# Kernel optimization log

Measured on AMD Instinct MI355X. Metric: run time of the kernel, lower is better.

The kernel has to match this reference:

```python
import jax, jax.numpy as jnp
import numpy as np

ALPHA = 0.2  # LeakyReLU negative slope
NEG_BIG = jnp.float32(-9e15)


def _leaky_relu(x):
    return jnp.where(x > 0, x, ALPHA * x)


def gat_layer(h, adj, w, a):
    """One GATLayer with concat=True (ELU output), dropout=0 (eval mode).
    h: [N, F_in], adj: [N, N] int, w: [F_in, F_out], a: [2*F_out, 1].
    """
    Wh = h @ w                         # [N, F_out]
    f_out = w.shape[1]
    Wh1 = Wh @ a[:f_out]               # [N, 1]
    Wh2 = Wh @ a[f_out:]               # [N, 1]
    e = _leaky_relu(Wh1 + Wh2.T)       # [N, N] dense additive scores
    att = jnp.where(adj > 0, e, NEG_BIG)
    att = jax.nn.softmax(att, axis=1)  # row softmax
    return jax.nn.elu(att @ Wh)        # [N, F_out]


def setup_inputs() -> dict:
    N, F_IN, H, NHEADS = 4096, 128, 64, 4
    key = jax.random.key(0)
    ks = jax.random.split(key, 9)
    s = jnp.float32(0.1)  # keep logits in a sane range
    x = jax.random.normal(ks[0], (N, F_IN), jnp.float32)
    adj = jax.random.randint(ks[1], (N, N), 0, 2, jnp.int32)
    return {
        "x": x,
        "adj": adj,
        "w_heads": jax.random.normal(ks[2], (NHEADS, F_IN, H), jnp.float32) * s,
        "a_heads": jax.random.normal(ks[3], (NHEADS, 2 * H, 1), jnp.float32) * s,
        "w_out": jax.random.normal(ks[4], (NHEADS * H, H), jnp.float32) * s,
        "a_out": jax.random.normal(ks[5], (2 * H, 1), jnp.float32) * s,
        "lin_w": jax.random.normal(ks[6], (H, F_IN), jnp.float32) * s,
        "lin_b": jnp.zeros((H,), jnp.float32),
        "outlin_w": jax.random.normal(ks[7], (H, H), jnp.float32) * s,
        "outlin_b": jnp.zeros((H,), jnp.float32),
    }


def reference(x, adj, w_heads, a_heads, w_out, a_out, lin_w, lin_b, outlin_w, outlin_b):
    N = x.shape[0]
    x_residual = x @ lin_w.T + lin_b                      # nn.Linear(input, hidden)
    # multi-head GAT layers, concatenated along features
    heads = jax.vmap(gat_layer, in_axes=(None, None, 0, 0))(x, adj, w_heads, a_heads)  # [nh, N, H]
    hcat = jnp.transpose(heads, (1, 0, 2)).reshape(N, -1)  # [N, nh*H]
    out = gat_layer(hcat, adj, w_out, a_out)               # out_att (concat=True => ELU)
    out = (x_residual + out) @ outlin_w.T + outlin_b       # out_linear
    return jax.nn.elu(out)
```

## Files before the change

### kernel.cpp

```cpp
#include <hip/hip_runtime.h>
#include <hip/hip_bf16.h>
#include <stdint.h>

#define F_IN 128
#define H 64
#define NH 4
#define KCH_H 16
#define KCH_O 32
#define LOG2E 1.44269504088896f

typedef __attribute__((ext_vector_type(8))) short bf16x8;
typedef __attribute__((ext_vector_type(4))) float floatx4;

static __device__ __forceinline__ unsigned short f2bf(float v) {
    __hip_bfloat16 b = __float2bfloat16(v);
    return *(unsigned short*)&b;
}
static __device__ __forceinline__ float bf2f(unsigned short u) {
    return __uint_as_float((unsigned int)u << 16);
}

__global__ void prep_kernel(const int* __restrict__ adj,
                            unsigned char* __restrict__ adjp,
                            const float* __restrict__ x,
                            const float* __restrict__ w_heads,
                            const float* __restrict__ a_heads,
                            const float* __restrict__ lin_w,
                            const float* __restrict__ lin_b,
                            unsigned short* __restrict__ Bpk,
                            float* __restrict__ x_res,
                            float* __restrict__ s1h,
                            float* __restrict__ s2h, int N) {
    const int bid = blockIdx.x;
    const int tid = threadIdx.x;
    const int KT = N >> 5;
    const int WH_BLOCKS = N / 8;

    if (bid >= WH_BLOCKS) {
        int idx = bid - WH_BLOCKS;
        int it = idx >> 3, rem = idx & 7, half = rem >> 2, zz = rem & 3;
        int i0 = it * 16;
        int n = tid & 15, q = (tid >> 4) & 3, w = tid >> 6;
        const int* row = adj + (size_t)(i0 + n) * N;
        unsigned char* dst = adjp + (size_t)it * KT * 64;
        int ktbase = half * (KT / 2) + zz * 16 + w;
#pragma unroll
        for (int j = 0; j < 4; ++j) {
            int kt = ktbase + 4 * j;
            int c0 = kt * 32 + q * 8;
            int4 a = *(const int4*)(row + c0);
            int4 b = *(const int4*)(row + c0 + 4);
            unsigned byte =
                (unsigned)(a.x > 0) | ((unsigned)(a.y > 0) << 1) |
                ((unsigned)(a.z > 0) << 2) | ((unsigned)(a.w > 0) << 3) |
                ((unsigned)(b.x > 0) << 4) | ((unsigned)(b.y > 0) << 5) |
                ((unsigned)(b.z > 0) << 6) | ((unsigned)(b.w > 0) << 7);
            dst[kt * 64 + q * 16 + n] = (unsigned char)byte;
        }
        return;
    }

    int h = tid >> 6, f = tid & 63;
    int i0 = bid * 8;
    __shared__ float xs[8][F_IN];
    __shared__ float lwT[F_IN][65];
    for (int e = tid; e < 8 * F_IN; e += 256)
        xs[e >> 7][e & 127] = x[(size_t)(i0 + (e >> 7)) * F_IN + (e & 127)];
    for (int e = tid; e < 64 * F_IN; e += 256) {
        int ff = e >> 7, k = e & 127;
        lwT[k][ff] = lin_w[e];
    }
    __syncthreads();
    float acc[8];
#pragma unroll
    for (int r = 0; r < 8; ++r) acc[r] = 0.f;
    float xr0 = 0.f, xr1 = 0.f;
    const float* w = w_heads + (size_t)h * F_IN * H + f;
#pragma unroll 4
    for (int k = 0; k < F_IN; ++k) {
        float wv = w[(size_t)k * H];
#pragma unroll
        for (int r = 0; r < 8; ++r) acc[r] += xs[r][k] * wv;
        float wx = lwT[k][f];
        xr0 += xs[h][k] * wx;
        xr1 += xs[h + 4][k] * wx;
    }
    {
        int kt = i0 >> 5, qq = (i0 >> 3) & 3;
        union { unsigned short s[8]; uint4 v; } t;
#pragma unroll
        for (int r = 0; r < 8; ++r) t.s[r] = f2bf(acc[r]);
        unsigned short* d = Bpk +
            (((size_t)(h * KT + kt) * 4 + (f >> 4)) * 64 + qq * 16 + (f & 15)) * 8;
        *(uint4*)d = t.v;
    }
    float b = lin_b[f];
    x_res[(size_t)(i0 + h) * H + f] = xr0 + b;
    x_res[(size_t)(i0 + h + 4) * H + f] = xr1 + b;
    float a1v = a_heads[(size_t)h * 2 * H + f];
    float a2v = a_heads[(size_t)h * 2 * H + H + f];
#pragma unroll
    for (int r = 0; r < 8; ++r) {
        float t1 = acc[r] * a1v;
        float t2 = acc[r] * a2v;
#pragma unroll
        for (int off = 32; off > 0; off >>= 1) {
            t1 += __shfl_xor(t1, off, 64);
            t2 += __shfl_xor(t2, off, 64);
        }
        if (f == 0) {
            s1h[(size_t)h * N + i0 + r] = t1 * LOG2E;
            s2h[(size_t)h * N + i0 + r] = t2 * LOG2E;
        }
    }
}

template <int KTC>
__global__ __launch_bounds__(256, 8)
void pv2_kernel(const unsigned char* __restrict__ adjp,
                const unsigned short* __restrict__ Bpk,
                const float* __restrict__ s1a,
                const float* __restrict__ s2a,
                unsigned short* __restrict__ outp, float* __restrict__ lp,
                int out_stride, int N) {
    const int h = blockIdx.y, z = blockIdx.z;
    const int KT = N >> 5;
    const int kt0 = z * KTC;
    const int tid = threadIdx.x;
    const int wave = tid >> 6, lane = tid & 63;
    const int n = lane & 15, q = lane >> 4;
    const int i0w = (blockIdx.x * 4 + wave) * 16;

    __shared__ float s2s[KTC * 32];
    __shared__ unsigned short ldsB[2][2048];
    __shared__ float lds_l[64];

    const float4* s2src = (const float4*)(s2a + (size_t)h * N + kt0 * 32);
    for (int e = tid; e < KTC * 8; e += 256) ((float4*)s2s)[e] = s2src[e];

    const unsigned short* Bb = Bpk + ((size_t)h * KT + kt0) * 2048;
    uint4 breg = *(const uint4*)(Bb + tid * 8);
    *(uint4*)&ldsB[0][tid * 8] = breg;
    breg = *(const uint4*)(Bb + 2048 + tid * 8);

    const unsigned char* ap = adjp + ((size_t)(i0w >> 4) * KT + kt0) * 64 + lane;
    unsigned int a_c = ap[0];
    unsigned int a_n = ap[64];
    const float s1v = s1a[(size_t)h * N + i0w + n];

    floatx4 acc[4];
    floatx4 accl = {0.f, 0.f, 0.f, 0.f};
#pragma unroll
    for (int g = 0; g < 4; ++g) acc[g] = (floatx4){0.f, 0.f, 0.f, 0.f};

    bf16x8 ones;
    {
        short one = (n == 0) ? (short)0x3F80 : (short)0;
#pragma unroll
        for (int jj = 0; jj < 8; ++jj) ones[jj] = one;
    }

    __syncthreads();

#pragma unroll 2
    for (int k = 0; k < KTC; ++k) {
        if (k + 1 < KTC) *(uint4*)&ldsB[(k + 1) & 1][tid * 8] = breg;
        unsigned int a_2 = 0;
        if (k + 2 < KTC) {
            breg = *(const uint4*)(Bb + (size_t)(k + 2) * 2048 + tid * 8);
            a_2 = ap[(size_t)(k + 2) * 64];
        }

        float4 sa = *(const float4*)&s2s[k * 32 + q * 8];
        float4 sb = *(const float4*)&s2s[k * 32 + q * 8 + 4];
        const float* sv = (const float*)&sa;
        const float* sw = (const float*)&sb;
        float e[8];
#pragma unroll
        for (int jj = 0; jj < 8; ++jj) {
            float sj = (jj < 4 ? sv[jj] : sw[jj - 4]);
            float tt = s1v + sj;
            float lr = fmaxf(tt, 0.2f * tt);
            lr = (a_c & (1u << jj)) ? lr : -150.f;
            e[jj] = __builtin_amdgcn_exp2f(lr);
        }
        union { unsigned int u[4]; bf16x8 v; } u;
        u.u[0] = __builtin_amdgcn_perm(__float_as_uint(e[1]), __float_as_uint(e[0]), 0x07060302u);
        u.u[1] = __builtin_amdgcn_perm(__float_as_uint(e[3]), __float_as_uint(e[2]), 0x07060302u);
        u.u[2] = __builtin_amdgcn_perm(__float_as_uint(e[5]), __float_as_uint(e[4]), 0x07060302u);
        u.u[3] = __builtin_amdgcn_perm(__float_as_uint(e[7]), __float_as_uint(e[6]), 0x07060302u);

        bf16x8 bf0 = *(const bf16x8*)&ldsB[k & 1][0 * 512 + lane * 8];
        bf16x8 bf1 = *(const bf16x8*)&ldsB[k & 1][1 * 512 + lane * 8];
        bf16x8 bf2 = *(const bf16x8*)&ldsB[k & 1][2 * 512 + lane * 8];
        bf16x8 bf3 = *(const bf16x8*)&ldsB[k & 1][3 * 512 + lane * 8];

        acc[0] = __builtin_amdgcn_mfma_f32_16x16x32_bf16(u.v, bf0, acc[0], 0, 0, 0);
        acc[1] = __builtin_amdgcn_mfma_f32_16x16x32_bf16(u.v, bf1, acc[1], 0, 0, 0);
        acc[2] = __builtin_amdgcn_mfma_f32_16x16x32_bf16(u.v, bf2, acc[2], 0, 0, 0);
        acc[3] = __builtin_amdgcn_mfma_f32_16x16x32_bf16(u.v, bf3, acc[3], 0, 0, 0);
        accl   = __builtin_amdgcn_mfma_f32_16x16x32_bf16(u.v, ones, accl, 0, 0, 0);

        a_c = a_n;
        a_n = a_2;
        __syncthreads();
    }

    unsigned short* lw = ((unsigned short*)ldsB) + wave * 1024;
#pragma unroll
    for (int r = 0; r < 4; ++r) {
        int row = q * 4 + r;
#pragma unroll
        for (int g = 0; g < 4; ++g)
            lw[row * 64 + g * 16 + n] = f2bf(acc[g][r]);
    }
    if (n == 0) {
#pragma unroll
        for (int r = 0; r < 4; ++r) lds_l[wave * 16 + q * 4 + r] = accl[r];
    }
    __syncthreads();
    unsigned short* obase = outp + ((size_t)z * N + i0w) * out_stride + h * 64;
#pragma unroll
    for (int j = 0; j < 2; ++j) {
        int c = j * 64 + lane;
        int row = c >> 3, ci = c & 7;
        *(uint4*)(obase + (size_t)row * out_stride + ci * 8) =
            *(const uint4*)(lw + row * 64 + ci * 8);
    }
    if (tid < 64) {
        float* lrow = lp + ((size_t)z * gridDim.y + h) * N + blockIdx.x * 64;
        lrow[tid] = lds_l[tid];
    }
}

__global__ void whout2_kernel(const unsigned short* __restrict__ hcp,
                              const float* __restrict__ lhp,
                              const float* __restrict__ w_out,
                              const float* __restrict__ a_out,
                              unsigned short* __restrict__ BpkO,
                              float* __restrict__ s1o,
                              float* __restrict__ s2o, int N) {
    int tid = threadIdx.x;
    int i0 = blockIdx.x * 8;
    int KT = N >> 5;
    __shared__ float hs[8][256];
    __shared__ float linv[8][NH];
    if (tid < 8 * NH) {
        int r = tid >> 2, hd = tid & 3;
        float l = 0.f;
#pragma unroll
        for (int p = 0; p < KCH_H; ++p)
            l += lhp[((size_t)p * NH + hd) * N + i0 + r];
        linv[r][hd] = 1.f / fmaxf(l, 1e-30f);
    }
    __syncthreads();
    const size_t ps = (size_t)N * 256;
    for (int e4 = tid; e4 < 8 * 64; e4 += 256) {
        int r = e4 >> 6, k4 = (e4 & 63) * 4;
        size_t off = (size_t)(i0 + r) * 256 + k4;
        float v0 = 0.f, v1 = 0.f, v2 = 0.f, v3 = 0.f;
#pragma unroll
        for (int p = 0; p < KCH_H; ++p) {
            ushort4 u = *(const ushort4*)(hcp + p * ps + off);
            v0 += bf2f(u.x); v1 += bf2f(u.y); v2 += bf2f(u.z); v3 += bf2f(u.w);
        }
        float li = linv[r][k4 >> 6];
        v0 *= li; v1 *= li; v2 *= li; v3 *= li;
        hs[r][k4]     = v0 > 0.f ? v0 : expm1f(v0);
        hs[r][k4 + 1] = v1 > 0.f ? v1 : expm1f(v1);
        hs[r][k4 + 2] = v2 > 0.f ? v2 : expm1f(v2);
        hs[r][k4 + 3] = v3 > 0.f ? v3 : expm1f(v3);
    }
    __syncthreads();
    int f = tid & 63, rl = tid >> 6;
    float a0 = 0.f, a1 = 0.f;
#pragma unroll 4
    for (int k = 0; k < 256; ++k) {
        float wv = w_out[(size_t)k * H + f];
        a0 += hs[rl][k] * wv;
        a1 += hs[rl + 4][k] * wv;
    }
    float w1 = a_out[f], w2 = a_out[H + f];
    float t10 = a0 * w1, t20 = a0 * w2, t11 = a1 * w1, t21 = a1 * w2;
#pragma unroll
    for (int off = 32; off > 0; off >>= 1) {
        t10 += __shfl_xor(t10, off, 64);
        t20 += __shfl_xor(t20, off, 64);
        t11 += __shfl_xor(t11, off, 64);
        t21 += __shfl_xor(t21, off, 64);
    }
    if (f == 0) {
        s1o[i0 + rl] = t10 * LOG2E;
        s2o[i0 + rl] = t20 * LOG2E;
        s1o[i0 + rl + 4] = t11 * LOG2E;
        s2o[i0 + rl + 4] = t21 * LOG2E;
    }
    __syncthreads();
    float* wsW = &hs[0][0];
    wsW[rl * 64 + f] = a0;
    wsW[(rl + 4) * 64 + f] = a1;
    __syncthreads();
    if (tid < 64) {
        int kt = i0 >> 5, qq = (i0 >> 3) & 3;
        int g = tid >> 4, nn = tid & 15;
        union { unsigned short s[8]; uint4 v; } t;
#pragma unroll
        for (int r = 0; r < 8; ++r) t.s[r] = f2bf(wsW[r * 64 + g * 16 + nn]);
        unsigned short* d = BpkO +
            (((size_t)kt * 4 + g) * 64 + qq * 16 + nn) * 8;
        *(uint4*)d = t.v;
    }
}

__global__ void final2_kernel(const unsigned short* __restrict__ o2p,
                              const float* __restrict__ lop,
                              const float* __restrict__ x_res,
                              const float* __restrict__ outlin_w,
                              const float* __restrict__ outlin_b,
                              float* __restrict__ out, int N) {
    int tid = threadIdx.x;
    int f = tid & 63, rl = tid >> 6;
    int i0 = blockIdx.x * 8;
    __shared__ float hs[8][H];
    __shared__ float linv[8];
    if (tid < 8) {
        float l = 0.f;
#pragma unroll
        for (int p = 0; p < KCH_O; ++p) l += lop[(size_t)p * N + i0 + tid];
        linv[tid] = 1.f / fmaxf(l, 1e-30f);
    }
    __syncthreads();
    const size_t ps = (size_t)N * 64;
    if (tid < 8 * 16) {
        int r = tid >> 4, f4 = (tid & 15) * 4;
        size_t off = (size_t)(i0 + r) * 64 + f4;
        float v0 = 0.f, v1 = 0.f, v2 = 0.f, v3 = 0.f;
#pragma unroll
        for (int p = 0; p < KCH_O; ++p) {
            ushort4 u = *(const ushort4*)(o2p + p * ps + off);
            v0 += bf2f(u.x); v1 += bf2f(u.y); v2 += bf2f(u.z); v3 += bf2f(u.w);
        }
        float li = linv[r];
        v0 *= li; v1 *= li; v2 *= li; v3 *= li;
        v0 = v0 > 0.f ? v0 : expm1f(v0);
        v1 = v1 > 0.f ? v1 : expm1f(v1);
        v2 = v2 > 0.f ? v2 : expm1f(v2);
        v3 = v3 > 0.f ? v3 : expm1f(v3);
        const float* xr = x_res + off;
        hs[r][f4]     = v0 + xr[0];
        hs[r][f4 + 1] = v1 + xr[1];
        hs[r][f4 + 2] = v2 + xr[2];
        hs[r][f4 + 3] = v3 + xr[3];
    }
    __syncthreads();
    float b = outlin_b[f];
    float a0 = b, a1 = b;
#pragma unroll 8
    for (int k = 0; k < H; ++k) {
        float wv = outlin_w[(size_t)f * H + k];
        a0 += hs[rl][k] * wv;
        a1 += hs[rl + 4][k] * wv;
    }
    a0 = a0 > 0.f ? a0 : expm1f(a0);
    a1 = a1 > 0.f ? a1 : expm1f(a1);
    out[(size_t)(i0 + rl) * H + f] = a0;
    out[(size_t)(i0 + rl + 4) * H + f] = a1;
}

extern "C" void kernel_launch(void* const* d_in, const int* in_sizes, int n_in,
                              void* d_out, int out_size, void* d_ws, size_t ws_size,
                              hipStream_t stream) {
    const float* x        = (const float*)d_in[0];
    const int*   adj      = (const int*)d_in[1];
    const float* w_heads  = (const float*)d_in[2];
    const float* a_heads  = (const float*)d_in[3];
    const float* w_out    = (const float*)d_in[4];
    const float* a_out    = (const float*)d_in[5];
    const float* lin_w    = (const float*)d_in[6];
    const float* lin_b    = (const float*)d_in[7];
    const float* outlin_w = (const float*)d_in[8];
    const float* outlin_b = (const float*)d_in[9];
    float* out = (float*)d_out;

    const int N = in_sizes[0] / F_IN;
    const int KT = N >> 5;

    char* p = (char*)d_ws;
    unsigned short* part = (unsigned short*)p;  p += (size_t)KCH_H * N * 256 * 2;
    float* x_res  = (float*)p;  p += (size_t)N * 64 * 4;
    float* s1h    = (float*)p;  p += (size_t)NH * N * 4;
    float* s2h    = (float*)p;  p += (size_t)NH * N * 4;
    float* s1o    = (float*)p;  p += (size_t)N * 4;
    float* s2o    = (float*)p;  p += (size_t)N * 4;
    float* lh_part = (float*)p; p += (size_t)KCH_H * NH * N * 4;
    float* lo_part = (float*)p; p += (size_t)KCH_O * N * 4;
    unsigned short* Bpk  = (unsigned short*)p;  p += (size_t)NH * KT * 2048 * 2;
    unsigned short* BpkO = (unsigned short*)p;  p += (size_t)KT * 2048 * 2;
    unsigned char* adjp  = (unsigned char*)p;   p += (size_t)(N / 16) * KT * 64;

    prep_kernel<<<N / 8 + (N / 16) * 8, 256, 0, stream>>>(
        adj, adjp, x, w_heads, a_heads, lin_w, lin_b, Bpk, x_res, s1h, s2h, N);
    pv2_kernel<8><<<dim3(N / 64, NH, KCH_H), 256, 0, stream>>>(
        adjp, Bpk, s1h, s2h, part, lh_part, NH * H, N);
    whout2_kernel<<<N / 8, 256, 0, stream>>>(part, lh_part, w_out, a_out,
                                             BpkO, s1o, s2o, N);
    pv2_kernel<4><<<dim3(N / 64, 1, KCH_O), 256, 0, stream>>>(
        adjp, BpkO, s1o, s2o, part, lo_part, H, N);
    final2_kernel<<<N / 8, 256, 0, stream>>>(part, lo_part, x_res, outlin_w, outlin_b, out, N);
}
```

Baseline: 192.4 us.

## Preload all B tiles and adjacency bits upfront, drop per-iteration barriers

```diff
diff --git a/kernel.cpp b/kernel.cpp
--- a/kernel.cpp
+++ b/kernel.cpp
@@ -115,9 +115,9 @@
     }
 }
 
-template <int KTC>
-__global__ __launch_bounds__(256, 8)
-void pv2_kernel(const unsigned char* __restrict__ adjp,
+template <int KTC, int MINW>
+__global__ __launch_bounds__(256, MINW)
+void pv5_kernel(const unsigned char* __restrict__ adjp,
                 const unsigned short* __restrict__ Bpk,
                 const float* __restrict__ s1a,
                 const float* __restrict__ s2a,
@@ -132,20 +132,20 @@
     const int i0w = (blockIdx.x * 4 + wave) * 16;
 
     __shared__ float s2s[KTC * 32];
-    __shared__ unsigned short ldsB[2][2048];
+    __shared__ unsigned short ldsB[KTC][2048];
     __shared__ float lds_l[64];
 
     const float4* s2src = (const float4*)(s2a + (size_t)h * N + kt0 * 32);
     for (int e = tid; e < KTC * 8; e += 256) ((float4*)s2s)[e] = s2src[e];
-
-    const unsigned short* Bb = Bpk + ((size_t)h * KT + kt0) * 2048;
-    uint4 breg = *(const uint4*)(Bb + tid * 8);
-    *(uint4*)&ldsB[0][tid * 8] = breg;
-    breg = *(const uint4*)(Bb + 2048 + tid * 8);
+    const unsigned short* Bb = Bpk + ((size_t)h * KT + kt0) * 2048 + tid * 8;
+#pragma unroll
+    for (int t = 0; t < KTC; ++t)
+        *(uint4*)&ldsB[t][tid * 8] = *(const uint4*)(Bb + (size_t)t * 2048);
 
     const unsigned char* ap = adjp + ((size_t)(i0w >> 4) * KT + kt0) * 64 + lane;
-    unsigned int a_c = ap[0];
-    unsigned int a_n = ap[64];
+    unsigned int a_all[KTC];
+#pragma unroll
+    for (int t = 0; t < KTC; ++t) a_all[t] = ap[(size_t)t * 64];
     const float s1v = s1a[(size_t)h * N + i0w + n];
 
     floatx4 acc[4];
@@ -162,15 +162,8 @@
 
     __syncthreads();
 
-#pragma unroll 2
+#pragma unroll
     for (int k = 0; k < KTC; ++k) {
-        if (k + 1 < KTC) *(uint4*)&ldsB[(k + 1) & 1][tid * 8] = breg;
-        unsigned int a_2 = 0;
-        if (k + 2 < KTC) {
-            breg = *(const uint4*)(Bb + (size_t)(k + 2) * 2048 + tid * 8);
-            a_2 = ap[(size_t)(k + 2) * 64];
-        }
-
         float4 sa = *(const float4*)&s2s[k * 32 + q * 8];
         float4 sb = *(const float4*)&s2s[k * 32 + q * 8 + 4];
         const float* sv = (const float*)&sa;
@@ -181,7 +174,7 @@
             float sj = (jj < 4 ? sv[jj] : sw[jj - 4]);
             float tt = s1v + sj;
             float lr = fmaxf(tt, 0.2f * tt);
-            lr = (a_c & (1u << jj)) ? lr : -150.f;
+            lr = (a_all[k] & (1u << jj)) ? lr : -150.f;
             e[jj] = __builtin_amdgcn_exp2f(lr);
         }
         union { unsigned int u[4]; bf16x8 v; } u;
@@ -190,22 +183,19 @@
         u.u[2] = __builtin_amdgcn_perm(__float_as_uint(e[5]), __float_as_uint(e[4]), 0x07060302u);
         u.u[3] = __builtin_amdgcn_perm(__float_as_uint(e[7]), __float_as_uint(e[6]), 0x07060302u);
 
-        bf16x8 bf0 = *(const bf16x8*)&ldsB[k & 1][0 * 512 + lane * 8];
-        bf16x8 bf1 = *(const bf16x8*)&ldsB[k & 1][1 * 512 + lane * 8];
-        bf16x8 bf2 = *(const bf16x8*)&ldsB[k & 1][2 * 512 + lane * 8];
-        bf16x8 bf3 = *(const bf16x8*)&ldsB[k & 1][3 * 512 + lane * 8];
+        bf16x8 bf0 = *(const bf16x8*)&ldsB[k][0 * 512 + lane * 8];
+        bf16x8 bf1 = *(const bf16x8*)&ldsB[k][1 * 512 + lane * 8];
+        bf16x8 bf2 = *(const bf16x8*)&ldsB[k][2 * 512 + lane * 8];
+        bf16x8 bf3 = *(const bf16x8*)&ldsB[k][3 * 512 + lane * 8];
 
         acc[0] = __builtin_amdgcn_mfma_f32_16x16x32_bf16(u.v, bf0, acc[0], 0, 0, 0);
         acc[1] = __builtin_amdgcn_mfma_f32_16x16x32_bf16(u.v, bf1, acc[1], 0, 0, 0);
         acc[2] = __builtin_amdgcn_mfma_f32_16x16x32_bf16(u.v, bf2, acc[2], 0, 0, 0);
         acc[3] = __builtin_amdgcn_mfma_f32_16x16x32_bf16(u.v, bf3, acc[3], 0, 0, 0);
         accl   = __builtin_amdgcn_mfma_f32_16x16x32_bf16(u.v, ones, accl, 0, 0, 0);
-
-        a_c = a_n;
-        a_n = a_2;
-        __syncthreads();
-    }
-
+    }
+
+    __syncthreads();
     unsigned short* lw = ((unsigned short*)ldsB) + wave * 1024;
 #pragma unroll
     for (int r = 0; r < 4; ++r) {
@@ -400,11 +390,11 @@
 
     prep_kernel<<<N / 8 + (N / 16) * 8, 256, 0, stream>>>(
         adj, adjp, x, w_heads, a_heads, lin_w, lin_b, Bpk, x_res, s1h, s2h, N);
-    pv2_kernel<8><<<dim3(N / 64, NH, KCH_H), 256, 0, stream>>>(
+    pv5_kernel<8, 4><<<dim3(N / 64, NH, KCH_H), 256, 0, stream>>>(
         adjp, Bpk, s1h, s2h, part, lh_part, NH * H, N);
     whout2_kernel<<<N / 8, 256, 0, stream>>>(part, lh_part, w_out, a_out,
                                              BpkO, s1o, s2o, N);
-    pv2_kernel<4><<<dim3(N / 64, 1, KCH_O), 256, 0, stream>>>(
+    pv5_kernel<4, 8><<<dim3(N / 64, 1, KCH_O), 256, 0, stream>>>(
         adjp, BpkO, s1o, s2o, part, lo_part, H, N);
     final2_kernel<<<N / 8, 256, 0, stream>>>(part, lo_part, x_res, outlin_w, outlin_b, out, N);
 }
```

Measured after the change: 202.6 us. +5.3%, slower.

## Factor exp of LeakyReLU scores into precomputed per-node exponentials

Applied to the files above, without the earlier changes.

```diff
diff --git a/kernel.cpp b/kernel.cpp
--- a/kernel.cpp
+++ b/kernel.cpp
@@ -29,8 +29,9 @@
                             const float* __restrict__ lin_b,
                             unsigned short* __restrict__ Bpk,
                             float* __restrict__ x_res,
-                            float* __restrict__ s1h,
-                            float* __restrict__ s2h, int N) {
+                            float* __restrict__ E1h, float* __restrict__ F1h,
+                            float* __restrict__ E2h, float* __restrict__ F2h,
+                            int N) {
     const int bid = blockIdx.x;
     const int tid = threadIdx.x;
     const int KT = N >> 5;
@@ -109,8 +110,12 @@
             t2 += __shfl_xor(t2, off, 64);
         }
         if (f == 0) {
-            s1h[(size_t)h * N + i0 + r] = t1 * LOG2E;
-            s2h[(size_t)h * N + i0 + r] = t2 * LOG2E;
+            float s1 = t1 * LOG2E, s2 = t2 * LOG2E;
+            size_t o = (size_t)h * N + i0 + r;
+            E1h[o] = __builtin_amdgcn_exp2f(s1);
+            F1h[o] = __builtin_amdgcn_exp2f(0.2f * s1);
+            E2h[o] = __builtin_amdgcn_exp2f(s2);
+            F2h[o] = __builtin_amdgcn_exp2f(0.2f * s2);
         }
     }
 }
@@ -119,8 +124,8 @@
 __global__ __launch_bounds__(256, 8)
 void pv2_kernel(const unsigned char* __restrict__ adjp,
                 const unsigned short* __restrict__ Bpk,
-                const float* __restrict__ s1a,
-                const float* __restrict__ s2a,
+                const float* __restrict__ E1a, const float* __restrict__ F1a,
+                const float* __restrict__ E2a, const float* __restrict__ F2a,
                 unsigned short* __restrict__ outp, float* __restrict__ lp,
                 int out_stride, int N) {
     const int h = blockIdx.y, z = blockIdx.z;
@@ -131,12 +136,17 @@
     const int n = lane & 15, q = lane >> 4;
     const int i0w = (blockIdx.x * 4 + wave) * 16;
 
-    __shared__ float s2s[KTC * 32];
+    __shared__ float e2s[KTC * 32];
+    __shared__ float f2s[KTC * 32];
     __shared__ unsigned short ldsB[2][2048];
     __shared__ float lds_l[64];
 
-    const float4* s2src = (const float4*)(s2a + (size_t)h * N + kt0 * 32);
-    for (int e = tid; e < KTC * 8; e += 256) ((float4*)s2s)[e] = s2src[e];
+    const float4* e2src = (const float4*)(E2a + (size_t)h * N + kt0 * 32);
+    const float4* f2src = (const float4*)(F2a + (size_t)h * N + kt0 * 32);
+    for (int e = tid; e < KTC * 8; e += 256) {
+        ((float4*)e2s)[e] = e2src[e];
+        ((float4*)f2s)[e] = f2src[e];
+    }
 
     const unsigned short* Bb = Bpk + ((size_t)h * KT + kt0) * 2048;
     uint4 breg = *(const uint4*)(Bb + tid * 8);
@@ -146,7 +156,8 @@
     const unsigned char* ap = adjp + ((size_t)(i0w >> 4) * KT + kt0) * 64 + lane;
     unsigned int a_c = ap[0];
     unsigned int a_n = ap[64];
-    const float s1v = s1a[(size_t)h * N + i0w + n];
+    const float E1v = E1a[(size_t)h * N + i0w + n];
+    const float F1v = F1a[(size_t)h * N + i0w + n];
 
     floatx4 acc[4];
     floatx4 accl = {0.f, 0.f, 0.f, 0.f};
@@ -171,18 +182,21 @@
             a_2 = ap[(size_t)(k + 2) * 64];
         }
 
-        float4 sa = *(const float4*)&s2s[k * 32 + q * 8];
-        float4 sb = *(const float4*)&s2s[k * 32 + q * 8 + 4];
-        const float* sv = (const float*)&sa;
-        const float* sw = (const float*)&sb;
+        float4 ea = *(const float4*)&e2s[k * 32 + q * 8];
+        float4 eb = *(const float4*)&e2s[k * 32 + q * 8 + 4];
+        float4 fa = *(const float4*)&f2s[k * 32 + q * 8];
+        float4 fb = *(const float4*)&f2s[k * 32 + q * 8 + 4];
+        const float* ev = (const float*)&ea;
+        const float* ew = (const float*)&eb;
+        const float* fv = (const float*)&fa;
+        const float* fw = (const float*)&fb;
         float e[8];
 #pragma unroll
         for (int jj = 0; jj < 8; ++jj) {
-            float sj = (jj < 4 ? sv[jj] : sw[jj - 4]);
-            float tt = s1v + sj;
-            float lr = fmaxf(tt, 0.2f * tt);
-            lr = (a_c & (1u << jj)) ? lr : -150.f;
-            e[jj] = __builtin_amdgcn_exp2f(lr);
+            float Ej = (jj < 4 ? ev[jj] : ew[jj - 4]);
+            float Fj = (jj < 4 ? fv[jj] : fw[jj - 4]);
+            float m = fmaxf(E1v * Ej, F1v * Fj);
+            e[jj] = (a_c & (1u << jj)) ? m : 0.f;
         }
         union { unsigned int u[4]; bf16x8 v; } u;
         u.u[0] = __builtin_amdgcn_perm(__float_as_uint(e[1]), __float_as_uint(e[0]), 0x07060302u);
@@ -238,8 +252,9 @@
                               const float* __restrict__ w_out,
                               const float* __restrict__ a_out,
                               unsigned short* __restrict__ BpkO,
-                              float* __restrict__ s1o,
-                              float* __restrict__ s2o, int N) {
+                              float* __restrict__ E1o, float* __restrict__ F1o,
+                              float* __restrict__ E2o, float* __restrict__ F2o,
+                              int N) {
     int tid = threadIdx.x;
     int i0 = blockIdx.x * 8;
     int KT = N >> 5;
@@ -290,10 +305,19 @@
         t21 += __shfl_xor(t21, off, 64);
     }
     if (f == 0) {
-        s1o[i0 + rl] = t10 * LOG2E;
-        s2o[i0 + rl] = t20 * LOG2E;
-        s1o[i0 + rl + 4] = t11 * LOG2E;
-        s2o[i0 + rl + 4] = t21 * LOG2E;
+        float s;
+        s = t10 * LOG2E;
+        E1o[i0 + rl] = __builtin_amdgcn_exp2f(s);
+        F1o[i0 + rl] = __builtin_amdgcn_exp2f(0.2f * s);
+        s = t20 * LOG2E;
+        E2o[i0 + rl] = __builtin_amdgcn_exp2f(s);
+        F2o[i0 + rl] = __builtin_amdgcn_exp2f(0.2f * s);
+        s = t11 * LOG2E;
+        E1o[i0 + rl + 4] = __builtin_amdgcn_exp2f(s);
+        F1o[i0 + rl + 4] = __builtin_amdgcn_exp2f(0.2f * s);
+        s = t21 * LOG2E;
+        E2o[i0 + rl + 4] = __builtin_amdgcn_exp2f(s);
+        F2o[i0 + rl + 4] = __builtin_amdgcn_exp2f(0.2f * s);
     }
     __syncthreads();
     float* wsW = &hs[0][0];
@@ -388,10 +412,14 @@
     char* p = (char*)d_ws;
     unsigned short* part = (unsigned short*)p;  p += (size_t)KCH_H * N * 256 * 2;
     float* x_res  = (float*)p;  p += (size_t)N * 64 * 4;
-    float* s1h    = (float*)p;  p += (size_t)NH * N * 4;
-    float* s2h    = (float*)p;  p += (size_t)NH * N * 4;
-    float* s1o    = (float*)p;  p += (size_t)N * 4;
-    float* s2o    = (float*)p;  p += (size_t)N * 4;
+    float* E1h    = (float*)p;  p += (size_t)NH * N * 4;
+    float* F1h    = (float*)p;  p += (size_t)NH * N * 4;
+    float* E2h    = (float*)p;  p += (size_t)NH * N * 4;
+    float* F2h    = (float*)p;  p += (size_t)NH * N * 4;
+    float* E1o    = (float*)p;  p += (size_t)N * 4;
+    float* F1o    = (float*)p;  p += (size_t)N * 4;
+    float* E2o    = (float*)p;  p += (size_t)N * 4;
+    float* F2o    = (float*)p;  p += (size_t)N * 4;
     float* lh_part = (float*)p; p += (size_t)KCH_H * NH * N * 4;
     float* lo_part = (float*)p; p += (size_t)KCH_O * N * 4;
     unsigned short* Bpk  = (unsigned short*)p;  p += (size_t)NH * KT * 2048 * 2;
@@ -399,12 +427,13 @@
     unsigned char* adjp  = (unsigned char*)p;   p += (size_t)(N / 16) * KT * 64;
 
     prep_kernel<<<N / 8 + (N / 16) * 8, 256, 0, stream>>>(
-        adj, adjp, x, w_heads, a_heads, lin_w, lin_b, Bpk, x_res, s1h, s2h, N);
+        adj, adjp, x, w_heads, a_heads, lin_w, lin_b, Bpk, x_res,
+        E1h, F1h, E2h, F2h, N);
     pv2_kernel<8><<<dim3(N / 64, NH, KCH_H), 256, 0, stream>>>(
-        adjp, Bpk, s1h, s2h, part, lh_part, NH * H, N);
+        adjp, Bpk, E1h, F1h, E2h, F2h, part, lh_part, NH * H, N);
     whout2_kernel<<<N / 8, 256, 0, stream>>>(part, lh_part, w_out, a_out,
-                                             BpkO, s1o, s2o, N);
+                                             BpkO, E1o, F1o, E2o, F2o, N);
     pv2_kernel<4><<<dim3(N / 64, 1, KCH_O), 256, 0, stream>>>(
-        adjp, BpkO, s1o, s2o, part, lo_part, H, N);
+        adjp, BpkO, E1o, F1o, E2o, F2o, part, lo_part, H, N);
     final2_kernel<<<N / 8, 256, 0, stream>>>(part, lo_part, x_res, outlin_w, outlin_b, out, N);
 }
```

After: 198.0 us. 2.9% more time.
